# Kernel tuning notes

Measured on AMD Instinct MI355X. Metric: run time of the kernel, lower is better.

## Reference

```python
import jax, jax.numpy as jnp
import numpy as np

V, WD, H, B, S, A = 50000, 300, 300, 64, 128, 8
H2 = 2 * H
NEG = -1e9


def _reverse_padded(x, lens):
    # reverse each sequence within its valid length; zeros elsewhere
    T = x.shape[1]
    idx = lens[:, None] - 1 - jnp.arange(T)[None, :]          # [B,T]
    valid = (idx >= 0)
    idx = jnp.clip(idx, 0, T - 1)
    return jnp.take_along_axis(x, idx[:, :, None], axis=1) * valid[:, :, None]


def _lstm_dir(x, lens, Wih, Whh, bih, bhh):
    # single-direction LSTM; emulates pack_padded: state frozen and output 0 past lens
    Bn, T, _ = x.shape
    Hn = Whh.shape[1]
    h0 = jnp.zeros((Bn, Hn), x.dtype)
    valid = (jnp.arange(T)[None, :] < lens[:, None]).astype(x.dtype)  # [B,T]

    def step(carry, inp):
        h, c = carry
        xt, vt = inp                                          # xt [B,D], vt [B,1]
        g = xt @ Wih.T + bih + h @ Whh.T + bhh                # [B,4H]
        i, f, gg, o = jnp.split(g, 4, axis=-1)                # torch gate order i,f,g,o
        i = jax.nn.sigmoid(i); f = jax.nn.sigmoid(f)
        o = jax.nn.sigmoid(o); gg = jnp.tanh(gg)
        c_new = f * c + i * gg
        h_new = o * jnp.tanh(c_new)
        h = vt * h_new + (1.0 - vt) * h
        c = vt * c_new + (1.0 - vt) * c
        return (h, c), vt * h_new

    _, outs = jax.lax.scan(step, (h0, h0), (x.transpose(1, 0, 2), valid.T[:, :, None]))
    return outs.transpose(1, 0, 2)                            # [B,T,H]


def _bilstm(x, lens, Wih, Whh, bih, bhh):
    fwd = _lstm_dir(x, lens, Wih[0], Whh[0], bih[0], bhh[0])
    xr = _reverse_padded(x, lens)
    bwd = _lstm_dir(xr, lens, Wih[1], Whh[1], bih[1], bhh[1])
    bwd = _reverse_padded(bwd, lens)
    return jnp.concatenate([fwd, bwd], axis=-1)               # [B,T,2H]


def setup_inputs() -> dict:
    key = jax.random.key(0)
    ks = jax.random.split(key, 16)
    lens_t = jax.random.randint(ks[0], (B,), S // 2, S + 1)
    ids_t = jax.random.randint(ks[1], (B, S), 1, V)
    text = jnp.where(jnp.arange(S)[None, :] < lens_t[:, None], ids_t, 0)
    lens_a = jax.random.randint(ks[2], (B,), 2, A + 1)
    ids_a = jax.random.randint(ks[3], (B, A), 1, V)
    aspect_ids = jnp.where(jnp.arange(A)[None, :] < lens_a[:, None], ids_a, 0)
    position_weight = jax.random.uniform(ks[4], (B, S), jnp.float32) * (text != 0)
    s = 0.05
    emb = jax.random.normal(ks[5], (V, WD), jnp.float32) * s
    emb = emb.at[0].set(0.0)  # padding row

    def lstm_params(k):
        k1, k2, k3, k4 = jax.random.split(k, 4)
        return (jax.random.normal(k1, (2, 4 * H, WD), jnp.float32) * s,
                jax.random.normal(k2, (2, 4 * H, H), jnp.float32) * s,
                jax.random.normal(k3, (2, 4 * H), jnp.float32) * s,
                jax.random.normal(k4, (2, 4 * H), jnp.float32) * s)

    l1_Wih, l1_Whh, l1_bih, l1_bhh = lstm_params(ks[6])
    l2_Wih, l2_Whh, l2_bih, l2_bhh = lstm_params(ks[7])
    return dict(
        text=text, aspect_ids=aspect_ids, position_weight=position_weight, emb=emb,
        l1_Wih=l1_Wih, l1_Whh=l1_Whh, l1_bih=l1_bih, l1_bhh=l1_bhh,
        l2_Wih=l2_Wih, l2_Whh=l2_Whh, l2_bih=l2_bih, l2_bhh=l2_bhh,
        lin1_W=jax.random.normal(ks[8], (2, H2, 2 * H2), jnp.float32) * s,
        lin1_b=jax.random.normal(ks[9], (2, H2), jnp.float32) * s,
        lin2_W=jax.random.normal(ks[10], (2, 1, H2), jnp.float32) * s,
        lin2_b=jax.random.normal(ks[11], (2, 1), jnp.float32) * s,
        fc_W=jax.random.normal(ks[12], (3, H2), jnp.float32) * s,
        fc_b=jax.random.normal(ks[13], (3,), jnp.float32) * s,
    )


def reference(text, aspect_ids, position_weight, emb,
              l1_Wih, l1_Whh, l1_bih, l1_bhh,
              l2_Wih, l2_Whh, l2_bih, l2_bhh,
              lin1_W, lin1_b, lin2_W, lin2_b, fc_W, fc_b):
    text_len = jnp.sum(text != 0, axis=-1)
    asp_len = jnp.sum(aspect_ids != 0, axis=-1)
    masks = (text != 0).astype(jnp.float32)          # [B,S]
    tmasks = (aspect_ids != 0).astype(jnp.float32)   # [B,A]
    wf = emb[text]                                    # [B,S,WD]
    af = emb[aspect_ids]                              # [B,A,WD]
    v = _bilstm(wf, text_len, l1_Wih, l1_Whh, l1_bih, l1_bhh)   # [B,S,2H]
    e = _bilstm(af, asp_len, l2_Wih, l2_Whh, l2_bih, l2_bhh)    # [B,A,2H]
    pair_mask = masks[:, :, None] * tmasks[:, None, :]          # [B,S,A]
    for i in range(2):
        a = jnp.einsum('bsd,bad->bsa', v, e)
        a = jnp.where(pair_mask == 0, NEG, a)
        a = jax.nn.softmax(a, axis=2)
        mid = jnp.einsum('bsa,bad->bsd', a, e)                  # [B,S,2H]
        mid = jnp.concatenate([mid, v], axis=-1)                # [B,S,4H]
        mid = jax.nn.leaky_relu(mid @ lin1_W[i].T + lin1_b[i])  # [B,S,2H]
        t = jax.nn.sigmoid(v @ lin2_W[i].T + lin2_b[i])         # [B,S,1]
        v = (1.0 - t) * mid + t * v
        v = position_weight[:, :, None] * v
    e_masked = jnp.where(tmasks[:, :, None] == 0, NEG, e)
    query = jnp.max(e_masked, axis=1)                           # [B,2H]
    alpha = jnp.einsum('bsd,bd->bs', v, query)
    alpha = jnp.where(masks == 0, NEG, alpha)
    alpha = jax.nn.softmax(alpha, axis=1)
    z = jnp.einsum('bs,bsd->bd', alpha, v)                      # [B,2H]
    return z @ fc_W.T + fc_b                                    # [B,3]
```

## Files before the change

### kernel.cpp

```cpp
#include <hip/hip_runtime.h>
#include <hip/hip_bf16.h>
#include <hip/hip_fp16.h>


typedef unsigned short u16;
typedef __attribute__((ext_vector_type(8))) short short8;
typedef __attribute__((ext_vector_type(4))) float floatx4;

#define NEGV -1e9f
#define MFMA __builtin_amdgcn_mfma_f32_16x16x32_bf16

__device__ __forceinline__ float bf2f(u16 u) {
    union { unsigned int i; float f; } x; x.i = ((unsigned int)u) << 16; return x.f;
}
__device__ __forceinline__ u16 f2bf(float f) {
    unsigned int u = __float_as_uint(f);
    unsigned int r = (u + 0x7fff + ((u >> 16) & 1)) >> 16;
    return (u16)r;
}
__device__ __forceinline__ float h16(u16 u) {
    __half h; *(u16*)&h = u; return __half2float(h);
}
__device__ __forceinline__ u16 f16(float f) {
    __half h = __float2half(f); return *(u16*)&h;
}
__device__ __forceinline__ float sigm(float x) { return 1.f / (1.f + expf(-x)); }
__device__ __forceinline__ float rdf(const void* p, size_t i, int flag) {
    return flag ? ((const float*)p)[i] : bf2f(((const u16*)p)[i]);
}

#if defined(__has_builtin)
# if __has_builtin(__builtin_amdgcn_fdot2)
#  define USE_FDOT2_BUILTIN 1
# endif
#endif
typedef __attribute__((ext_vector_type(2))) _Float16 half2v;
__device__ __forceinline__ float dot2f(unsigned int w, unsigned int h, float acc) {
#ifdef USE_FDOT2_BUILTIN
    union { unsigned int u; half2v v; } a, b;
    a.u = w; b.u = h;
    return __builtin_amdgcn_fdot2(a.v, b.v, acc, false);
#else
    asm("v_dot2_f32_f16 %0, %1, %2, %0" : "+v"(acc) : "v"(w), "v"(h));
    return acc;
#endif
}

__global__ void k_detect(const void* __restrict__ emb, int* __restrict__ flag) {
    __shared__ int cnt;
    if (threadIdx.x == 0) cnt = 0;
    __syncthreads();
    u16 x = ((const u16*)emb)[4096 + threadIdx.x];
    int e = (x >> 7) & 0xFF;
    if (e >= 0x8A) atomicAdd(&cnt, 1);
    __syncthreads();
    if (threadIdx.x == 0) *flag = (cnt > 8) ? 1 : 0;
}

__global__ __launch_bounds__(256) void k_prep_all(
    const int* __restrict__ text, const int* __restrict__ asp,
    int* __restrict__ lens, const int* __restrict__ flag,
    const void* __restrict__ W1ih, const void* __restrict__ W2ih,
    u16* __restrict__ d1h, u16* __restrict__ d1l,
    u16* __restrict__ d2h, u16* __restrict__ d2l,
    const void* __restrict__ W1hh, const void* __restrict__ W2hh,
    u16* __restrict__ dh1, u16* __restrict__ dh2,
    const void* pw, const void* l2w, const void* l2b,
    const void* fcw, const void* fcb, const void* lb,
    const void* b1i, const void* b1h, const void* b2i, const void* b2h,
    float* __restrict__ dst, float* __restrict__ bl,
    float* __restrict__ bt, float* __restrict__ ba)
{
    int blk = blockIdx.x;
    int tid = threadIdx.x;
    int f = *flag;
    if (blk < 6080) {
        int i = blk * 256 + tid;
        int layer = i / (2432 * 320), r = i - layer * (2432 * 320);
        int n = r / 320, k = r - n * 320;
        const void* W = layer ? W2ih : W1ih;
        float val = (n < 2400 && k < 300) ? rdf(W, (size_t)n * 300 + k, f) : 0.f;
        u16 hi = f2bf(val);
        float lo = val - bf2f(hi);
        if (layer) { d2h[r] = hi; d2l[r] = f2bf(lo); }
        else       { d1h[r] = hi; d1l[r] = f2bf(lo); }
    } else if (blk < 11705) {
        int i = (blk - 6080) * 256 + tid;
        int layer = i / 720000, r = i - layer * 720000;
        int dir = r / 360000, rr = r - dir * 360000;
        int kp = rr / 2400, t = rr - kp * 2400;
        int cc = t >> 1, j = t & 1;
        int k = 2 * kp + j;
        const void* W = layer ? W2hh : W1hh;
        u16 bits = f16(rdf(W, (size_t)dir * 360000 + (size_t)cc * 300 + k, f));
        if (layer) dh2[r] = bits; else dh1[r] = bits;
    } else if (blk < 11754) {
        int i = (blk - 11705) * 256 + tid;
        if (i < 8192)            dst[i] = rdf(pw, i, f);
        else if (i < 9392)       dst[i] = rdf(l2w, i - 8192, f);
        else if (i < 9394)       dst[i] = rdf(l2b, i - 9392, f);
        else if (i < 11194)      dst[i] = rdf(fcw, i - 9394, f);
        else if (i < 11197)      dst[i] = rdf(fcb, i - 11194, f);
        if (i < 1280) {
            int dir = i / 640, c = i - dir * 640;
            bl[i] = (c < 600) ? rdf(lb, dir * 600 + c, f) : 0.f;
        }
        if (i < 2400) {
            bt[i] = rdf(b1i, i, f) + rdf(b1h, i, f);
            ba[i] = rdf(b2i, i, f) + rdf(b2h, i, f);
        }
    } else {
        if (tid < 64) {
            int c = 0;
            for (int s = 0; s < 128; ++s) c += (text[tid * 128 + s] != 0);
            lens[tid] = c;
        } else if (tid < 128) {
            int b = tid - 64; int c = 0;
            for (int a = 0; a < 8; ++a) c += (asp[b * 8 + a] != 0);
            lens[64 + b] = c;
        }
    }
}

__device__ __forceinline__ void gemm_emb_tile(
    const void* __restrict__ emb, const int* __restrict__ ids,
    int base, int rpb, int stride, int f,
    const u16* __restrict__ Bhi, const u16* __restrict__ Blo,
    const float* __restrict__ bias,
    u16* __restrict__ C, int ldc, int nstore, int bx, int by, int tid)
{
    int wave = tid >> 6, lane = tid & 63;
    int l15 = lane & 15, quad = lane >> 4;
    int m0 = bx * 64 + wave * 16;
    int n0 = by * 64;

    int m = m0 + l15;
    int b = m / rpb, j = m - b * rpb;
    int id = ids[b * stride + base + j];
    const float* arow_f = (const float*)emb + (size_t)id * 300;
    const u16*   arow_b = (const u16*)emb + (size_t)id * 300;

    const u16* Bp  = Bhi + (size_t)(n0 + l15) * 320 + quad * 8;
    const u16* Bp2 = Blo + (size_t)(n0 + l15) * 320 + quad * 8;

    floatx4 acc0 = {0.f, 0.f, 0.f, 0.f};
    floatx4 acc1 = acc0, acc2 = acc0, acc3 = acc0;

    for (int kc = 0; kc < 10; ++kc) {
        int ko = kc * 32 + quad * 8;
        short8 ahi, alo;
        if (f) {
            if (ko + 8 <= 300) {
                float4 fa = *(const float4*)(arow_f + ko);
                float4 fb = *(const float4*)(arow_f + ko + 4);
                float vv[8] = {fa.x, fa.y, fa.z, fa.w, fb.x, fb.y, fb.z, fb.w};
                #pragma unroll
                for (int t = 0; t < 8; ++t) {
                    u16 h = f2bf(vv[t]);
                    ahi[t] = (short)h;
                    alo[t] = (short)f2bf(vv[t] - bf2f(h));
                }
            } else {
                #pragma unroll
                for (int t = 0; t < 8; ++t) {
                    int k = ko + t;
                    float vv = (k < 300) ? arow_f[k] : 0.f;
                    u16 h = f2bf(vv);
                    ahi[t] = (short)h;
                    alo[t] = (short)f2bf(vv - bf2f(h));
                }
            }
        } else {
            #pragma unroll
            for (int t = 0; t < 8; ++t) {
                int k = ko + t;
                ahi[t] = (k < 300) ? (short)arow_b[k] : (short)0;
                alo[t] = 0;
            }
        }
        int ko2 = kc * 32;
        short8 bh0 = *(const short8*)(Bp + ko2);
        short8 bh1 = *(const short8*)(Bp + (size_t)16 * 320 + ko2);
        short8 bh2 = *(const short8*)(Bp + (size_t)32 * 320 + ko2);
        short8 bh3 = *(const short8*)(Bp + (size_t)48 * 320 + ko2);
        short8 bl0 = *(const short8*)(Bp2 + ko2);
        short8 bl1 = *(const short8*)(Bp2 + (size_t)16 * 320 + ko2);
        short8 bl2 = *(const short8*)(Bp2 + (size_t)32 * 320 + ko2);
        short8 bl3 = *(const short8*)(Bp2 + (size_t)48 * 320 + ko2);
        acc0 = MFMA(ahi, bh0, acc0, 0, 0, 0);
        acc1 = MFMA(ahi, bh1, acc1, 0, 0, 0);
        acc2 = MFMA(ahi, bh2, acc2, 0, 0, 0);
        acc3 = MFMA(ahi, bh3, acc3, 0, 0, 0);
        acc0 = MFMA(ahi, bl0, acc0, 0, 0, 0);
        acc1 = MFMA(ahi, bl1, acc1, 0, 0, 0);
        acc2 = MFMA(ahi, bl2, acc2, 0, 0, 0);
        acc3 = MFMA(ahi, bl3, acc3, 0, 0, 0);
        acc0 = MFMA(alo, bh0, acc0, 0, 0, 0);
        acc1 = MFMA(alo, bh1, acc1, 0, 0, 0);
        acc2 = MFMA(alo, bh2, acc2, 0, 0, 0);
        acc3 = MFMA(alo, bh3, acc3, 0, 0, 0);
    }

    #pragma unroll
    for (int c = 0; c < 4; ++c) {
        floatx4 acc = (c == 0) ? acc0 : (c == 1) ? acc1 : (c == 2) ? acc2 : acc3;
        int col = n0 + c * 16 + l15;
        if (col >= nstore) continue;
        float bb = bias[col];
        #pragma unroll
        for (int r = 0; r < 4; ++r) {
            int row = m0 + quad * 4 + r;
            C[(size_t)row * ldc + col] = f16(acc[r] + bb);
        }
    }
}

__global__ __launch_bounds__(256) void k_gemm_emb3(
    const void* __restrict__ emb, const int* __restrict__ text,
    const int* __restrict__ asp, const int* __restrict__ flag,
    const u16* __restrict__ wiht_hi, const u16* __restrict__ wiht_lo,
    const u16* __restrict__ wiha_hi, const u16* __restrict__ wiha_lo,
    const float* __restrict__ bias_t, const float* __restrict__ bias_a,
    u16* __restrict__ xproj_a, u16* __restrict__ xf0, u16* __restrict__ xb0)
{
    int g = blockIdx.x;
    int f = *flag;
    if (g < 304) {
        int bx = g & 7, by = g >> 3;
        gemm_emb_tile(emb, asp, 0, 8, 8, f, wiha_hi, wiha_lo, bias_a,
                      xproj_a, 2400, 2400, bx, by, threadIdx.x);
    } else if (g < 912) {
        int t = g - 304; int bx = t & 31, by = t >> 5;
        gemm_emb_tile(emb, text, 0, 32, 128, f, wiht_hi, wiht_lo, bias_t,
                      xf0, 1200, 1200, bx, by, threadIdx.x);
    } else {
        int t = g - 912; int bx = t & 31, by = t >> 5;
        gemm_emb_tile(emb, text, 96, 32, 128, f,
                      wiht_hi + 1200ull * 320, wiht_lo + 1200ull * 320,
                      bias_t + 1200, xb0, 1200, 1200, bx, by, threadIdx.x);
    }
}

__device__ __forceinline__ void gemm_core(
    const u16* __restrict__ Ap, const u16* __restrict__ Ap2,
    const u16* __restrict__ Bp, const u16* __restrict__ Bp2,
    int lda, int ldb, int nk,
    floatx4& acc0, floatx4& acc1, floatx4& acc2, floatx4& acc3)
{
    for (int kc = 0; kc < nk; ++kc) {
        int ko = kc * 32;
        short8 bh0 = *(const short8*)(Bp + ko);
        short8 bh1 = *(const short8*)(Bp + (size_t)16 * ldb + ko);
        short8 bh2 = *(const short8*)(Bp + (size_t)32 * ldb + ko);
        short8 bh3 = *(const short8*)(Bp + (size_t)48 * ldb + ko);
        short8 bl0 = *(const short8*)(Bp2 + ko);
        short8 bl1 = *(const short8*)(Bp2 + (size_t)16 * ldb + ko);
        short8 bl2 = *(const short8*)(Bp2 + (size_t)32 * ldb + ko);
        short8 bl3 = *(const short8*)(Bp2 + (size_t)48 * ldb + ko);
        short8 a  = *(const short8*)(Ap + ko);
        short8 al = *(const short8*)(Ap2 + ko);
        acc0 = MFMA(a, bh0, acc0, 0, 0, 0);
        acc1 = MFMA(a, bh1, acc1, 0, 0, 0);
        acc2 = MFMA(a, bh2, acc2, 0, 0, 0);
        acc3 = MFMA(a, bh3, acc3, 0, 0, 0);
        acc0 = MFMA(a, bl0, acc0, 0, 0, 0);
        acc1 = MFMA(a, bl1, acc1, 0, 0, 0);
        acc2 = MFMA(a, bl2, acc2, 0, 0, 0);
        acc3 = MFMA(a, bl3, acc3, 0, 0, 0);
        acc0 = MFMA(al, bh0, acc0, 0, 0, 0);
        acc1 = MFMA(al, bh1, acc1, 0, 0, 0);
        acc2 = MFMA(al, bh2, acc2, 0, 0, 0);
        acc3 = MFMA(al, bh3, acc3, 0, 0, 0);
    }
}

__global__ void k_esplit(const float* __restrict__ e,
                         u16* __restrict__ ehi, u16* __restrict__ elo) {
    int i = blockIdx.x * 256 + threadIdx.x;
    if (i >= 512 * 608) return;
    int r = i / 608, k = i - r * 608;
    float val = (k < 600) ? e[r * 600 + k] : 0.f;
    u16 h = f2bf(val);
    ehi[i] = h;
    elo[i] = f2bf(val - bf2f(h));
}

__global__ __launch_bounds__(256) void gemm_ew(
    const u16* __restrict__ Ahi, const u16* __restrict__ Alo,
    const u16* __restrict__ l1a_hi, const u16* __restrict__ l1a_lo,
    float* __restrict__ EW)
{
    int tid = threadIdx.x;
    int wave = tid >> 6, lane = tid & 63;
    int l15 = lane & 15, quad = lane >> 4;
    int iter = blockIdx.z;
    int m0 = blockIdx.x * 64 + wave * 16;
    int n0 = blockIdx.y * 64;
    const u16* Ap  = Ahi + (size_t)(m0 + l15) * 608 + quad * 8;
    const u16* Ap2 = Alo + (size_t)(m0 + l15) * 608 + quad * 8;
    const u16* Bp  = l1a_hi + (size_t)iter * 640 * 608 + (size_t)(n0 + l15) * 608 + quad * 8;
    const u16* Bp2 = l1a_lo + (size_t)iter * 640 * 608 + (size_t)(n0 + l15) * 608 + quad * 8;
    floatx4 acc0 = {0.f, 0.f, 0.f, 0.f};
    floatx4 acc1 = acc0, acc2 = acc0, acc3 = acc0;
    gemm_core(Ap, Ap2, Bp, Bp2, 608, 608, 19, acc0, acc1, acc2, acc3);
    #pragma unroll
    for (int c = 0; c < 4; ++c) {
        floatx4 acc = (c == 0) ? acc0 : (c == 1) ? acc1 : (c == 2) ? acc2 : acc3;
        int col = n0 + c * 16 + l15;
        if (col >= 600) continue;
        #pragma unroll
        for (int r = 0; r < 4; ++r) {
            int row = m0 + quad * 4 + r;
            EW[((size_t)iter * 512 + row) * 600 + col] = acc[r];
        }
    }
}

__global__ __launch_bounds__(256) void gemm_vt(
    const u16* __restrict__ vhi, const u16* __restrict__ vlo,
    const u16* __restrict__ Bhi, const u16* __restrict__ Blo,
    const float* __restrict__ bias,
    const float* __restrict__ EW, const float* __restrict__ a_sm,
    const float* __restrict__ tg, const float* __restrict__ pw,
    float* __restrict__ vio)
{
    __shared__ float al_s[64][8];
    __shared__ float ew_s[8][64];
    int tid = threadIdx.x;
    int wave = tid >> 6, lane = tid & 63;
    int l15 = lane & 15, quad = lane >> 4;
    int m0 = blockIdx.x * 64 + wave * 16;
    int n0 = blockIdx.y * 64;
    int row0 = blockIdx.x * 64;
    int bidx = row0 >> 7;

    for (int i = tid; i < 512; i += 256)
        al_s[i >> 3][i & 7] = a_sm[(size_t)(row0 + (i >> 3)) * 8 + (i & 7)];
    for (int i = tid; i < 512; i += 256) {
        int a = i >> 6, cc = i & 63;
        int col = n0 + cc;
        ew_s[a][cc] = (col < 600) ? EW[((size_t)bidx * 8 + a) * 600 + col] : 0.f;
    }
    __syncthreads();

    const u16* Ap  = vhi + (size_t)(m0 + l15) * 608 + quad * 8;
    const u16* Ap2 = vlo + (size_t)(m0 + l15) * 608 + quad * 8;
    const u16* Bp  = Bhi + (size_t)(n0 + l15) * 608 + quad * 8;
    const u16* Bp2 = Blo + (size_t)(n0 + l15) * 608 + quad * 8;
    floatx4 acc0 = {0.f, 0.f, 0.f, 0.f};
    floatx4 acc1 = acc0, acc2 = acc0, acc3 = acc0;
    gemm_core(Ap, Ap2, Bp, Bp2, 608, 608, 19, acc0, acc1, acc2, acc3);

    #pragma unroll
    for (int c = 0; c < 4; ++c) {
        floatx4 acc = (c == 0) ? acc0 : (c == 1) ? acc1 : (c == 2) ? acc2 : acc3;
        int cc = c * 16 + l15;
        int col = n0 + cc;
        if (col >= 600) continue;
        float bb = bias[col];
        #pragma unroll
        for (int r = 0; r < 4; ++r) {
            int rr = wave * 16 + quad * 4 + r;
            int row = row0 + rr;
            float mid = 0.f;
            #pragma unroll
            for (int a = 0; a < 8; ++a) mid += al_s[rr][a] * ew_s[a][cc];
            float val = acc[r] + bb + mid;
            val = val > 0.f ? val : 0.01f * val;
            float t = tg[row];
            size_t vi = (size_t)row * 600 + col;
            float vv = vio[vi];
            vio[vi] = pw[row] * ((1.f - t) * val + t * vv);
        }
    }
}

__global__ __launch_bounds__(960, 1) void k_lstm6(
    const u16* __restrict__ xf, const u16* __restrict__ xb, int ldx, int rpb,
    int base_f, int base_b, const u16* __restrict__ whhT,
    const int* __restrict__ lens, float* __restrict__ out, int T, int init,
    float* __restrict__ hst, float* __restrict__ cst, int nsteps,
    const u16* __restrict__ xa, const u16* __restrict__ whhA,
    const int* __restrict__ lensA, float* __restrict__ outA,
    float* __restrict__ hstA, float* __restrict__ cstA, int nLstm,
    const void* __restrict__ emb, const int* __restrict__ text,
    int bf_next, int bb_next, const int* __restrict__ flag,
    const u16* __restrict__ wih_hi, const u16* __restrict__ wih_lo,
    const float* __restrict__ bias_t,
    u16* __restrict__ xf_next, u16* __restrict__ xb_next,
    int nGemm, int fmode, const int* __restrict__ aspF,
    float* __restrict__ queryF, const void* __restrict__ lin1W,
    u16* __restrict__ l1a_hi, u16* __restrict__ l1a_lo,
    u16* __restrict__ l1b_hi, u16* __restrict__ l1b_lo)
{
    __shared__ float part[6][1200];
    __shared__ u16 wlds[6][4][2400];
    __shared__ __align__(4) u16 hs16[304];
    int blk = blockIdx.x;
    if (blk >= nLstm + nGemm) {
        int fb = blk - nLstm - nGemm;
        int i = fb * 960 + threadIdx.x;
        if (fmode == 1) {
            if (i < 64 * 600) {
                int b = i / 600, d = i - b * 600;
                float m = NEGV;
                for (int a = 0; a < 8; ++a)
                    if (aspF[b * 8 + a] != 0)
                        m = fmaxf(m, outA[(size_t)b * 4800 + a * 600 + d]);
                queryF[i] = m;
            }
        } else {
            if (i < 2 * 640 * 608) {
                int f = *flag;
                int it = i / (640 * 608), r = i - it * (640 * 608);
                int n = r / 608, k = r - n * 608;
                float va = 0.f, vb = 0.f;
                if (n < 600 && k < 600) {
                    va = rdf(lin1W, (size_t)it * 720000 + (size_t)n * 1200 + k, f);
                    vb = rdf(lin1W, (size_t)it * 720000 + (size_t)n * 1200 + 600 + k, f);
                }
                u16 h;
                h = f2bf(va); l1a_hi[i] = h; l1a_lo[i] = f2bf(va - bf2f(h));
                h = f2bf(vb); l1b_hi[i] = h; l1b_lo[i] = f2bf(vb - bf2f(h));
            }
        }
        return;
    }
    if (blk >= nLstm) {
        if (threadIdx.x >= 256) return;
        int g = blk - nLstm;
        int dirn = g / 608; int t = g - dirn * 608;
        int bx = t & 31, by = t >> 5;
        gemm_emb_tile(emb, text, dirn ? bb_next : bf_next, 32, 128, *flag,
                      wih_hi + (dirn ? 1200ull * 320 : 0),
                      wih_lo + (dirn ? 1200ull * 320 : 0),
                      bias_t + (dirn ? 1200 : 0),
                      dirn ? xb_next : xf_next, 1200, 1200, bx, by, threadIdx.x);
        return;
    }
    if (blk >= 128) {
        blk -= 128;
        xf = xa; xb = xa + 1200; ldx = 2400; rpb = 8;
        base_f = 0; base_b = 0;
        whhT = whhA; lens = lensA; out = outA; T = 8; init = 1;
        hst = hstA; cst = cstA; nsteps = 8;
    }
    int tid = threadIdx.x;
    int g6 = tid / 160, u = tid - g6 * 160;
    bool act = (u < 150);
    int b = blk >> 1, dir = blk & 1;
    int len = lens[b];
    float c = 0.f, hf = 0.f;
    const u16* wbase = whhT + (size_t)dir * 360000 + (size_t)g6 * 60000 + 16 * u;

    uint4 wA[8], wB[8];
    if (act) {
        #pragma unroll
        for (int r = 0; r < 8; ++r) {
            wA[r] = *(const uint4*)(wbase + (size_t)r * 2400);
            wB[r] = *(const uint4*)(wbase + (size_t)r * 2400 + 8);
        }
        #pragma unroll
        for (int r = 0; r < 4; ++r) {
            *(uint4*)&wlds[g6][r][16 * u]     = *(const uint4*)(wbase + (size_t)(8 + r) * 2400);
            *(uint4*)&wlds[g6][r][16 * u + 8] = *(const uint4*)(wbase + (size_t)(8 + r) * 2400 + 8);
        }
    }
    if (tid < 300) {
        hf = init ? 0.f : hst[(size_t)blk * 300 + tid];
        c  = init ? 0.f : cst[(size_t)blk * 300 + tid];
        hs16[tid] = f16(hf);
    }
    __syncthreads();
    const u16* wstream = wbase + (size_t)12 * 2400;

    for (int s = 0; s < nsteps; ++s) {
        int pos = dir ? (base_b + nsteps - 1 - s) : (base_f + s);
        if (pos >= len) continue;
        if (act) {
            float a0 = 0.f, a1 = 0.f, a2 = 0.f, a3 = 0.f;
            float a4 = 0.f, a5 = 0.f, a6 = 0.f, a7 = 0.f;
            const unsigned int* h2p = (const unsigned int*)(hs16 + g6 * 50);
            #define DOT8(va, vb, hh)                                   \
                a0 = dot2f((va).x, hh, a0); a1 = dot2f((va).y, hh, a1);\
                a2 = dot2f((va).z, hh, a2); a3 = dot2f((va).w, hh, a3);\
                a4 = dot2f((vb).x, hh, a4); a5 = dot2f((vb).y, hh, a5);\
                a6 = dot2f((vb).z, hh, a6); a7 = dot2f((vb).w, hh, a7);
            #pragma unroll
            for (int r = 0; r < 8; ++r) {
                unsigned int h2 = h2p[r];
                DOT8(wA[r], wB[r], h2);
            }
            #pragma unroll
            for (int r = 0; r < 4; ++r) {
                unsigned int h2 = h2p[8 + r];
                uint4 va = *(const uint4*)&wlds[g6][r][16 * u];
                uint4 vb = *(const uint4*)&wlds[g6][r][16 * u + 8];
                DOT8(va, vb, h2);
            }
            const u16* wp = wstream;
            #pragma unroll 4
            for (int i = 0; i < 13; ++i) {
                unsigned int h2 = h2p[12 + i];
                uint4 va = *(const uint4*)wp;
                uint4 vb = *(const uint4*)(wp + 8);
                wp += 2400;
                DOT8(va, vb, h2);
            }
            #undef DOT8
            float* pp = &part[g6][8 * u];
            float4 w0 = {a0, a1, a2, a3};
            float4 w1 = {a4, a5, a6, a7};
            *(float4*)pp = w0;
            *(float4*)(pp + 4) = w1;
        }
        __syncthreads();
        if (tid < 300) {
            const u16* xr = dir ? (xb + (size_t)(b * rpb + pos - base_b) * ldx)
                                : (xf + (size_t)(b * rpb + pos - base_f) * ldx);
            float gi = h16(xr[tid]), gf = h16(xr[300 + tid]);
            float gg = h16(xr[600 + tid]), go = h16(xr[900 + tid]);
            #pragma unroll
            for (int g = 0; g < 6; ++g) {
                gi += part[g][tid];
                gf += part[g][300 + tid];
                gg += part[g][600 + tid];
                go += part[g][900 + tid];
            }
            gi = sigm(gi); gf = sigm(gf); gg = tanhf(gg); go = sigm(go);
            c = gf * c + gi * gg;
            float hn = go * tanhf(c);
            out[((size_t)b * T + pos) * 600 + dir * 300 + tid] = hn;
            hf = hn;
            hs16[tid] = f16(hn);
        }
        __syncthreads();
    }
    if (tid < 300) {
        hst[(size_t)blk * 300 + tid] = hf;
        cst[(size_t)blk * 300 + tid] = c;
    }
}

__global__ __launch_bounds__(128) void k_scorev(
    const float* __restrict__ v, const float* __restrict__ e,
    const int* __restrict__ text, const int* __restrict__ asp,
    const float* __restrict__ l2w, const float* __restrict__ l2b, int iter,
    float* __restrict__ a_sm, float* __restrict__ tg,
    u16* __restrict__ vhi, u16* __restrict__ vlo)
{
    __shared__ float vs[600];
    __shared__ float red[2][9];
    int row = blockIdx.x;
    int b = row >> 7;
    int t = threadIdx.x, wv = t >> 6, lane = t & 63;
    const float* vrow = v + (size_t)row * 600;
    const float* eb = e + (size_t)b * 4800;
    const float* w2 = l2w + iter * 600;

    for (int d = t; d < 600; d += 128) vs[d] = vrow[d];
    __syncthreads();

    float acc[9];
    #pragma unroll
    for (int j = 0; j < 9; ++j) acc[j] = 0.f;
    for (int d = t; d < 600; d += 128) {
        float vv = vs[d];
        #pragma unroll
        for (int a = 0; a < 8; ++a) acc[a] += vv * eb[a * 600 + d];
        acc[8] += vv * w2[d];
    }
    #pragma unroll
    for (int off = 32; off >= 1; off >>= 1) {
        #pragma unroll
        for (int j = 0; j < 9; ++j) acc[j] += __shfl_down(acc[j], off, 64);
    }
    if (lane == 0) {
        #pragma unroll
        for (int j = 0; j < 9; ++j) red[wv][j] = acc[j];
    }
    __syncthreads();
    if (t == 0) {
        float dots[9];
        #pragma unroll
        for (int j = 0; j < 9; ++j) dots[j] = red[0][j] + red[1][j];
        tg[row] = sigm(dots[8] + l2b[iter]);
        bool sm = (text[row] != 0);
        float sc[8]; float mx = -INFINITY;
        #pragma unroll
        for (int a = 0; a < 8; ++a) {
            sc[a] = (sm && asp[b * 8 + a] != 0) ? dots[a] : NEGV;
            mx = fmaxf(mx, sc[a]);
        }
        float den = 0.f;
        #pragma unroll
        for (int a = 0; a < 8; ++a) { sc[a] = expf(sc[a] - mx); den += sc[a]; }
        float inv = 1.f / den;
        #pragma unroll
        for (int a = 0; a < 8; ++a) a_sm[(size_t)row * 8 + a] = sc[a] * inv;
    }
    for (int d = t; d < 608; d += 128) {
        float val = (d < 600) ? vs[d] : 0.f;
        u16 h = f2bf(val);
        vhi[(size_t)row * 608 + d] = h;
        vlo[(size_t)row * 608 + d] = f2bf(val - bf2f(h));
    }
}

__global__ __launch_bounds__(128) void k_final(
    const float* __restrict__ v, const float* __restrict__ q,
    const int* __restrict__ text, const float* __restrict__ fcW,
    const float* __restrict__ fcb, const int* __restrict__ flag, void* __restrict__ outv)
{
    __shared__ float red[128];
    __shared__ float al[128];
    __shared__ float zz[600];
    __shared__ float qs[608];
    __shared__ float vt[128][33];
    int b = blockIdx.x, s = threadIdx.x;
    const float* vb = v + (size_t)b * 128 * 600;
    for (int d = s; d < 608; d += 128) qs[d] = (d < 600) ? q[(size_t)b * 600 + d] : 0.f;
    __syncthreads();
    float sc = 0.f;
    for (int d0 = 0; d0 < 600; d0 += 32) {
        #pragma unroll
        for (int k = 0; k < 4; ++k) {
            ;
        }
        for (int i = s; i < 128 * 32; i += 128) {
            int row = i >> 5, col = i & 31;
            int d = d0 + col;
            vt[row][col] = (d < 600) ? vb[(size_t)row * 600 + d] : 0.f;
        }
        __syncthreads();
        #pragma unroll
        for (int col = 0; col < 32; ++col)
            sc += vt[s][col] * qs[d0 + col];
        __syncthreads();
    }
    if (text[b * 128 + s] == 0) sc = NEGV;
    red[s] = sc; __syncthreads();
    for (int off = 64; off >= 1; off >>= 1) {
        if (s < off) red[s] = fmaxf(red[s], red[s + off]);
        __syncthreads();
    }
    float mx = red[0]; __syncthreads();
    float ex = expf(sc - mx);
    red[s] = ex; __syncthreads();
    for (int off = 64; off >= 1; off >>= 1) {
        if (s < off) red[s] += red[s + off];
        __syncthreads();
    }
    float alpha = ex / red[0];
    al[s] = alpha; __syncthreads();
    for (int d = s; d < 600; d += 128) {
        float z = 0.f;
        for (int s2 = 0; s2 < 128; ++s2) z += al[s2] * v[(size_t)(b * 128 + s2) * 600 + d];
        zz[d] = z;
    }
    __syncthreads();
    if (s < 3) {
        float o = 0.f;
        for (int d = 0; d < 600; ++d) o += zz[d] * fcW[s * 600 + d];
        o += fcb[s];
        if (*flag) ((float*)outv)[b * 3 + s] = o;
        else       ((u16*)outv)[b * 3 + s] = f2bf(o);
    }
}

extern "C" void kernel_launch(void* const* d_in, const int* in_sizes, int n_in,
                              void* d_out, int out_size, void* d_ws, size_t ws_size,
                              hipStream_t stream) {
    const int*  text   = (const int*)d_in[0];
    const int*  asp    = (const int*)d_in[1];
    const void* pw     = d_in[2];
    const void* emb    = d_in[3];
    const void* l1_Wih = d_in[4];
    const void* l1_Whh = d_in[5];
    const void* l1_bih = d_in[6];
    const void* l1_bhh = d_in[7];
    const void* l2_Wih = d_in[8];
    const void* l2_Whh = d_in[9];
    const void* l2_bih = d_in[10];
    const void* l2_bhh = d_in[11];
    const void* lin1_W = d_in[12];
    const void* lin1_b = d_in[13];
    const void* lin2_W = d_in[14];
    const void* lin2_b = d_in[15];
    const void* fcW    = d_in[16];
    const void* fcb    = d_in[17];
    (void)ws_size; (void)n_in; (void)in_sizes; (void)out_size;

    char* w = (char*)d_ws;
    size_t off = 0;
    auto alloc = [&](size_t bytes) -> void* {
        void* p = w + off;
        off += (bytes + 255) & ~(size_t)255;
        return p;
    };
    int*   flag     = (int*)  alloc(4);
    int*   lens     = (int*)  alloc(128ull * 4);
    float* bias_t   = (float*)alloc(2400ull * 4);
    float* bias_a   = (float*)alloc(2400ull * 4);
    float* bias_l1  = (float*)alloc(1280ull * 4);
    float* smallf   = (float*)alloc(11197ull * 4);
    float* tg       = (float*)alloc(8192ull * 4);
    float* a_sm     = (float*)alloc(8192ull * 8 * 4);
    float* query    = (float*)alloc(64ull * 600 * 4);
    float* hst_t    = (float*)alloc(128ull * 300 * 4);
    float* cst_t    = (float*)alloc(128ull * 300 * 4);
    float* hst_a    = (float*)alloc(128ull * 300 * 4);
    float* cst_a    = (float*)alloc(128ull * 300 * 4);
    float* e        = (float*)alloc(512ull * 600 * 4);
    float* v        = (float*)alloc(8192ull * 600 * 4);
    float* pw_f     = smallf;
    float* l2w_f    = smallf + 8192;
    float* l2b_f    = smallf + 9392;
    float* fcW_f    = smallf + 9394;
    float* fcb_f    = smallf + 11194;
    size_t phase_off = off;
    u16*   wiht_hi  = (u16*)  alloc(2432ull * 320 * 2);
    u16*   wiht_lo  = (u16*)  alloc(2432ull * 320 * 2);
    u16*   wiha_hi  = (u16*)  alloc(2432ull * 320 * 2);
    u16*   wiha_lo  = (u16*)  alloc(2432ull * 320 * 2);
    u16*   whhT_t   = (u16*)  alloc(720000ull * 2);
    u16*   whhT_a   = (u16*)  alloc(720000ull * 2);
    u16*   xf0      = (u16*)  alloc(2048ull * 1200 * 2);
    u16*   xb0      = (u16*)  alloc(2048ull * 1200 * 2);
    u16*   xf1      = (u16*)  alloc(2048ull * 1200 * 2);
    u16*   xb1      = (u16*)  alloc(2048ull * 1200 * 2);
    u16*   xproj_a  = (u16*)  alloc(512ull * 2400 * 2);
    off = phase_off;
    u16*   l1a_hi   = (u16*)  alloc(2ull * 640 * 608 * 2);
    u16*   l1a_lo   = (u16*)  alloc(2ull * 640 * 608 * 2);
    u16*   l1b_hi   = (u16*)  alloc(2ull * 640 * 608 * 2);
    u16*   l1b_lo   = (u16*)  alloc(2ull * 640 * 608 * 2);
    u16*   ehi      = (u16*)  alloc(512ull * 608 * 2);
    u16*   elo      = (u16*)  alloc(512ull * 608 * 2);
    float* EW       = (float*)alloc(2ull * 512 * 600 * 4);
    u16*   vhi      = (u16*)  alloc(8192ull * 608 * 2);
    u16*   vlo      = (u16*)  alloc(8192ull * 608 * 2);

    hipMemsetAsync(v, 0, 8192ull * 600 * 4, stream);
    hipMemsetAsync(e, 0, 512ull * 600 * 4, stream);

    k_detect<<<1, 256, 0, stream>>>(emb, flag);
    k_prep_all<<<11755, 256, 0, stream>>>(
        text, asp, lens, flag,
        l1_Wih, l2_Wih, wiht_hi, wiht_lo, wiha_hi, wiha_lo,
        l1_Whh, l2_Whh, whhT_t, whhT_a,
        pw, lin2_W, lin2_b, fcW, fcb, lin1_b,
        l1_bih, l1_bhh, l2_bih, l2_bhh,
        smallf, bias_l1, bias_t, bias_a);

    k_gemm_emb3<<<1520, 256, 0, stream>>>(
        emb, text, asp, flag, wiht_hi, wiht_lo, wiha_hi, wiha_lo,
        bias_t, bias_a, xproj_a, xf0, xb0);

    for (int kk = 0; kk < 4; ++kk) {
        int bf = 32 * kk;
        int bb = 96 - 32 * kk;
        u16* xfc = (kk & 1) ? xf1 : xf0;
        u16* xbc = (kk & 1) ? xb1 : xb0;
        u16* xfn = (kk & 1) ? xf0 : xf1;
        u16* xbn = (kk & 1) ? xb0 : xb1;
        int nLstm = (kk == 0) ? 256 : 128;
        int nGemm = (kk < 3) ? 1216 : 0;
        int fmode = (kk == 1) ? 1 : (kk == 3) ? 2 : 0;
        int nFuse = (kk == 1) ? 40 : (kk == 3) ? 811 : 0;
        int nblk = nLstm + nGemm + nFuse;
        k_lstm6<<<nblk, 960, 0, stream>>>(xfc, xbc, 1200, 32, bf, bb,
            whhT_t, lens, v, 128, kk == 0 ? 1 : 0, hst_t, cst_t, 32,
            xproj_a, whhT_a, lens + 64, e, hst_a, cst_a, nLstm,
            emb, text, bf + 32, bb - 32, flag, wiht_hi, wiht_lo, bias_t,
            xfn, xbn,
            nGemm, fmode, asp, query, lin1_W,
            l1a_hi, l1a_lo, l1b_hi, l1b_lo);
    }

    k_esplit<<<(512 * 608 + 255) / 256, 256, 0, stream>>>(e, ehi, elo);
    gemm_ew<<<dim3(8, 10, 2), 256, 0, stream>>>(ehi, elo, l1a_hi, l1a_lo, EW);

    for (int iter = 0; iter < 2; ++iter) {
        k_scorev<<<8192, 128, 0, stream>>>(v, e, text, asp, l2w_f, l2b_f,
            iter, a_sm, tg, vhi, vlo);
        gemm_vt<<<dim3(128, 10), 256, 0, stream>>>(vhi, vlo,
            l1b_hi + (size_t)iter * 640 * 608, l1b_lo + (size_t)iter * 640 * 608,
            bias_l1 + iter * 640, EW + (size_t)iter * 512 * 600,
            a_sm, tg, pw_f, v);
    }

    k_final<<<64, 128, 0, stream>>>(v, query, text, fcW_f, fcb_f, flag, d_out);
}
```

Measured before the change: 1.208 ms.

## Move lin1 padding and query out of LSTM kernel, split final into parallel kernels

The lin1 weight split/pad and the aspect-query max reduction leave the fused LSTM kernel and become standalone launches, so the LSTM launches carry fewer extra blocks. The 64-block final kernel is split into four kernels: query max, a per-row wave-reduced score, a 320-block softmax plus weighted sum, and a small FC reduction. This aims to expose more parallelism in the tail, where 64 blocks left most of the GPU idle. It adds several kernel launches and gives up the overlap of the side work with the serial LSTM recurrence.

```diff
diff --git a/kernel.cpp b/kernel.cpp
--- a/kernel.cpp
+++ b/kernel.cpp
@@ -122,6 +122,24 @@
     }
 }
 
+__global__ void k_pad_lin1AB(const void* __restrict__ W, const int* __restrict__ flag,
+                             u16* __restrict__ Ahi, u16* __restrict__ Alo,
+                             u16* __restrict__ Bhi, u16* __restrict__ Blo) {
+    int i = blockIdx.x * 256 + threadIdx.x;
+    if (i >= 2 * 640 * 608) return;
+    int f = *flag;
+    int it = i / (640 * 608), r = i - it * (640 * 608);
+    int n = r / 608, k = r - n * 608;
+    float va = 0.f, vb = 0.f;
+    if (n < 600 && k < 600) {
+        va = rdf(W, (size_t)it * 720000 + (size_t)n * 1200 + k, f);
+        vb = rdf(W, (size_t)it * 720000 + (size_t)n * 1200 + 600 + k, f);
+    }
+    u16 h;
+    h = f2bf(va); Ahi[i] = h; Alo[i] = f2bf(va - bf2f(h));
+    h = f2bf(vb); Bhi[i] = h; Blo[i] = f2bf(vb - bf2f(h));
+}
+
 __device__ __forceinline__ void gemm_emb_tile(
     const void* __restrict__ emb, const int* __restrict__ ids,
     int base, int rpb, int stride, int f,
@@ -387,45 +405,12 @@
     int bf_next, int bb_next, const int* __restrict__ flag,
     const u16* __restrict__ wih_hi, const u16* __restrict__ wih_lo,
     const float* __restrict__ bias_t,
-    u16* __restrict__ xf_next, u16* __restrict__ xb_next,
-    int nGemm, int fmode, const int* __restrict__ aspF,
-    float* __restrict__ queryF, const void* __restrict__ lin1W,
-    u16* __restrict__ l1a_hi, u16* __restrict__ l1a_lo,
-    u16* __restrict__ l1b_hi, u16* __restrict__ l1b_lo)
+    u16* __restrict__ xf_next, u16* __restrict__ xb_next)
 {
     __shared__ float part[6][1200];
     __shared__ u16 wlds[6][4][2400];
     __shared__ __align__(4) u16 hs16[304];
     int blk = blockIdx.x;
-    if (blk >= nLstm + nGemm) {
-        int fb = blk - nLstm - nGemm;
-        int i = fb * 960 + threadIdx.x;
-        if (fmode == 1) {
-            if (i < 64 * 600) {
-                int b = i / 600, d = i - b * 600;
-                float m = NEGV;
-                for (int a = 0; a < 8; ++a)
-                    if (aspF[b * 8 + a] != 0)
-                        m = fmaxf(m, outA[(size_t)b * 4800 + a * 600 + d]);
-                queryF[i] = m;
-            }
-        } else {
-            if (i < 2 * 640 * 608) {
-                int f = *flag;
-                int it = i / (640 * 608), r = i - it * (640 * 608);
-                int n = r / 608, k = r - n * 608;
-                float va = 0.f, vb = 0.f;
-                if (n < 600 && k < 600) {
-                    va = rdf(lin1W, (size_t)it * 720000 + (size_t)n * 1200 + k, f);
-                    vb = rdf(lin1W, (size_t)it * 720000 + (size_t)n * 1200 + 600 + k, f);
-                }
-                u16 h;
-                h = f2bf(va); l1a_hi[i] = h; l1a_lo[i] = f2bf(va - bf2f(h));
-                h = f2bf(vb); l1b_hi[i] = h; l1b_lo[i] = f2bf(vb - bf2f(h));
-            }
-        }
-        return;
-    }
     if (blk >= nLstm) {
         if (threadIdx.x >= 256) return;
         int g = blk - nLstm;
@@ -607,64 +592,95 @@
     }
 }
 
-__global__ __launch_bounds__(128) void k_final(
+__global__ void k_query(const float* __restrict__ e, const int* __restrict__ asp,
+                        float* __restrict__ q) {
+    int i = blockIdx.x * 256 + threadIdx.x;
+    if (i >= 64 * 600) return;
+    int b = i / 600, d = i - b * 600;
+    float m = NEGV;
+    for (int a = 0; a < 8; ++a)
+        if (asp[b * 8 + a] != 0) m = fmaxf(m, e[(size_t)b * 4800 + a * 600 + d]);
+    q[i] = m;
+}
+
+__global__ __launch_bounds__(256) void k_scoreq(
     const float* __restrict__ v, const float* __restrict__ q,
-    const int* __restrict__ text, const float* __restrict__ fcW,
-    const float* __restrict__ fcb, const int* __restrict__ flag, void* __restrict__ outv)
+    const int* __restrict__ text, float* __restrict__ sc)
+{
+    int row = blockIdx.x * 4 + (threadIdx.x >> 6);
+    int lane = threadIdx.x & 63;
+    int b = row >> 7;
+    const float* vr = v + (size_t)row * 600;
+    const float* qb = q + (size_t)b * 600;
+    float s = 0.f;
+    for (int d = lane; d < 600; d += 64) s += vr[d] * qb[d];
+    #pragma unroll
+    for (int off = 32; off >= 1; off >>= 1) s += __shfl_down(s, off, 64);
+    if (lane == 0) sc[row] = (text[row] == 0) ? NEGV : s;
+}
+
+__global__ __launch_bounds__(128) void k_zout(
+    const float* __restrict__ v, const float* __restrict__ sc,
+    float* __restrict__ z)
 {
     __shared__ float red[128];
     __shared__ float al[128];
-    __shared__ float zz[600];
-    __shared__ float qs[608];
-    __shared__ float vt[128][33];
-    int b = blockIdx.x, s = threadIdx.x;
-    const float* vb = v + (size_t)b * 128 * 600;
-    for (int d = s; d < 608; d += 128) qs[d] = (d < 600) ? q[(size_t)b * 600 + d] : 0.f;
+    int b = blockIdx.x / 5, chunk = blockIdx.x % 5;
+    int t = threadIdx.x;
+    float s = sc[b * 128 + t];
+    red[t] = s; __syncthreads();
+    for (int off = 64; off >= 1; off >>= 1) {
+        if (t < off) red[t] = fmaxf(red[t], red[t + off]);
+        __syncthreads();
+    }
+    float mx = red[0]; __syncthreads();
+    float ex = expf(s - mx);
+    red[t] = ex; __syncthreads();
+    for (int off = 64; off >= 1; off >>= 1) {
+        if (t < off) red[t] += red[t + off];
+        __syncthreads();
+    }
+    al[t] = ex / red[0];
     __syncthreads();
-    float sc = 0.f;
-    for (int d0 = 0; d0 < 600; d0 += 32) {
-        #pragma unroll
-        for (int k = 0; k < 4; ++k) {
-            ;
-        }
-        for (int i = s; i < 128 * 32; i += 128) {
-            int row = i >> 5, col = i & 31;
-            int d = d0 + col;
-            vt[row][col] = (d < 600) ? vb[(size_t)row * 600 + d] : 0.f;
+    int d = chunk * 120 + t;
+    if (t < 120) {
+        const float* vb = v + (size_t)b * 128 * 600 + d;
+        float zz = 0.f;
+        for (int s2 = 0; s2 < 128; ++s2)
+            zz += al[s2] * vb[(size_t)s2 * 600];
+        z[(size_t)b * 600 + d] = zz;
+    }
+}
+
+__global__ __launch_bounds__(128) void k_fc(
+    const float* __restrict__ z, const float* __restrict__ fcW,
+    const float* __restrict__ fcb, const int* __restrict__ flag,
+    void* __restrict__ outv)
+{
+    __shared__ float red[3][128];
+    int b = blockIdx.x, t = threadIdx.x;
+    const float* zb = z + (size_t)b * 600;
+    float p0 = 0.f, p1 = 0.f, p2 = 0.f;
+    for (int d = t; d < 600; d += 128) {
+        float zz = zb[d];
+        p0 += zz * fcW[d];
+        p1 += zz * fcW[600 + d];
+        p2 += zz * fcW[1200 + d];
+    }
+    red[0][t] = p0; red[1][t] = p1; red[2][t] = p2;
+    __syncthreads();
+    for (int off = 64; off >= 1; off >>= 1) {
+        if (t < off) {
+            red[0][t] += red[0][t + off];
+            red[1][t] += red[1][t + off];
+            red[2][t] += red[2][t + off];
         }
         __syncthreads();
-        #pragma unroll
-        for (int col = 0; col < 32; ++col)
-            sc += vt[s][col] * qs[d0 + col];
-        __syncthreads();
-    }
-    if (text[b * 128 + s] == 0) sc = NEGV;
-    red[s] = sc; __syncthreads();
-    for (int off = 64; off >= 1; off >>= 1) {
-        if (s < off) red[s] = fmaxf(red[s], red[s + off]);
-        __syncthreads();
-    }
-    float mx = red[0]; __syncthreads();
-    float ex = expf(sc - mx);
-    red[s] = ex; __syncthreads();
-    for (int off = 64; off >= 1; off >>= 1) {
-        if (s < off) red[s] += red[s + off];
-        __syncthreads();
-    }
-    float alpha = ex / red[0];
-    al[s] = alpha; __syncthreads();
-    for (int d = s; d < 600; d += 128) {
-        float z = 0.f;
-        for (int s2 = 0; s2 < 128; ++s2) z += al[s2] * v[(size_t)(b * 128 + s2) * 600 + d];
-        zz[d] = z;
-    }
-    __syncthreads();
-    if (s < 3) {
-        float o = 0.f;
-        for (int d = 0; d < 600; ++d) o += zz[d] * fcW[s * 600 + d];
-        o += fcb[s];
-        if (*flag) ((float*)outv)[b * 3 + s] = o;
-        else       ((u16*)outv)[b * 3 + s] = f2bf(o);
+    }
+    if (t < 3) {
+        float o = red[t][0] + fcb[t];
+        if (*flag) ((float*)outv)[b * 3 + t] = o;
+        else       ((u16*)outv)[b * 3 + t] = f2bf(o);
     }
 }
 
@@ -707,6 +723,8 @@
     float* tg       = (float*)alloc(8192ull * 4);
     float* a_sm     = (float*)alloc(8192ull * 8 * 4);
     float* query    = (float*)alloc(64ull * 600 * 4);
+    float* sc       = (float*)alloc(8192ull * 4);
+    float* z        = (float*)alloc(64ull * 600 * 4);
     float* hst_t    = (float*)alloc(128ull * 300 * 4);
     float* cst_t    = (float*)alloc(128ull * 300 * 4);
     float* hst_a    = (float*)alloc(128ull * 300 * 4);
@@ -765,19 +783,17 @@
         u16* xfn = (kk & 1) ? xf0 : xf1;
         u16* xbn = (kk & 1) ? xb0 : xb1;
         int nLstm = (kk == 0) ? 256 : 128;
-        int nGemm = (kk < 3) ? 1216 : 0;
-        int fmode = (kk == 1) ? 1 : (kk == 3) ? 2 : 0;
-        int nFuse = (kk == 1) ? 40 : (kk == 3) ? 811 : 0;
-        int nblk = nLstm + nGemm + nFuse;
+        int haveNext = (kk < 3);
+        int nblk = nLstm + (haveNext ? 1216 : 0);
         k_lstm6<<<nblk, 960, 0, stream>>>(xfc, xbc, 1200, 32, bf, bb,
             whhT_t, lens, v, 128, kk == 0 ? 1 : 0, hst_t, cst_t, 32,
             xproj_a, whhT_a, lens + 64, e, hst_a, cst_a, nLstm,
             emb, text, bf + 32, bb - 32, flag, wiht_hi, wiht_lo, bias_t,
-            xfn, xbn,
-            nGemm, fmode, asp, query, lin1_W,
-            l1a_hi, l1a_lo, l1b_hi, l1b_lo);
-    }
-
+            xfn, xbn);
+    }
+
+    k_pad_lin1AB<<<(2 * 640 * 608 + 255) / 256, 256, 0, stream>>>(
+        lin1_W, flag, l1a_hi, l1a_lo, l1b_hi, l1b_lo);
     k_esplit<<<(512 * 608 + 255) / 256, 256, 0, stream>>>(e, ehi, elo);
     gemm_ew<<<dim3(8, 10, 2), 256, 0, stream>>>(ehi, elo, l1a_hi, l1a_lo, EW);
 
@@ -790,5 +806,8 @@
             a_sm, tg, pw_f, v);
     }
 
-    k_final<<<64, 128, 0, stream>>>(v, query, text, fcW_f, fcb_f, flag, d_out);
-}
+    k_query<<<150, 256, 0, stream>>>(e, asp, query);
+    k_scoreq<<<2048, 256, 0, stream>>>(v, query, text, sc);
+    k_zout<<<320, 128, 0, stream>>>(v, sc, z);
+    k_fc<<<64, 128, 0, stream>>>(z, fcW_f, fcb_f, flag, d_out);
+}
```

Result: faster. 1.034 ms (-14.4%).
